# Performance work log

Hardware: AMD Instinct MI355X
Metric: run time of the kernel (lower is better)

The kernel has to match this reference:

```python
import jax, jax.numpy as jnp
import numpy as np

B, T, E, H = 2, 2048, 1024, 16  # batch, seq(block_size), n_embed, n_head


def setup_inputs() -> dict:
    key = jax.random.key(0)
    kx, kq, kk, kv, kf = jax.random.split(key, 5)
    s = 0.02
    return {
        "x": jax.random.normal(kx, (B, T, E), jnp.float32),
        "Wq": jax.random.normal(kq, (E, E), jnp.float32) * s,
        "Wk": jax.random.normal(kk, (E, E), jnp.float32) * s,
        "Wv": jax.random.normal(kv, (E, E), jnp.float32) * s,
        "Wf": jax.random.normal(kf, (E, E), jnp.float32) * s,
        "bf": jnp.zeros((E,), jnp.float32),
    }


def reference(x, Wq, Wk, Wv, Wf, bf):
    b, t, e = x.shape
    dh = e // H
    # per-head projections (no bias), heads concatenated along feature dim
    q = (x @ Wq).reshape(b, t, H, dh)
    k = (x @ Wk).reshape(b, t, H, dh)
    v = (x @ Wv).reshape(b, t, H, dh)
    # NOTE: original scales by sqrt(full embed dim C), not sqrt(head_size)
    scores = jnp.einsum("bqhd,bkhd->bhqk", q, k) / jnp.sqrt(jnp.asarray(e, x.dtype))
    causal = jnp.tril(jnp.ones((t, t), bool))
    scores = jnp.where(causal, scores, -jnp.inf)
    wei = jax.nn.softmax(scores, axis=-1)
    attn = jnp.einsum("bhqk,bkhd->bqhd", wei, v).reshape(b, t, e)
    x = x + attn  # residual (no out-projection in original)
    # FeedForward: single Linear + ReLU, residual
    return x + jnp.maximum(x @ Wf + bf, 0)
```

## Files before the change

### kernel.cpp

```cpp
#include <hip/hip_runtime.h>
#include <cstdint>
#include <cstddef>

typedef unsigned short u16;
typedef short short8 __attribute__((ext_vector_type(8)));
typedef float floatx4 __attribute__((ext_vector_type(4)));

__device__ __forceinline__ float bf2f(u16 u) {
    union { unsigned int i; float f; } v; v.i = ((unsigned int)u) << 16; return v.f;
}
__device__ __forceinline__ u16 f2bf(float f) {
    union { float f; unsigned int i; } v; v.f = f;
    unsigned int u = v.i;
    return (u16)((u + 0x7fffu + ((u >> 16) & 1u)) >> 16);
}

#if __has_builtin(__builtin_amdgcn_exp2f)
#define EXP2F(x) __builtin_amdgcn_exp2f(x)
#else
#define EXP2F(x) exp2f(x)
#endif

__device__ __forceinline__ void gload_lds16(const u16* g, void* lds_wave_base) {
    __builtin_amdgcn_global_load_lds(
        (__attribute__((address_space(1))) void*)g,
        (__attribute__((address_space(3))) void*)lds_wave_base,
        16, 0, 0);
}

__global__ void conv_transpose_k(const float* __restrict__ w0, const float* __restrict__ w1,
                                 const float* __restrict__ w2, const float* __restrict__ w3,
                                 u16* __restrict__ o0, u16* __restrict__ o1,
                                 u16* __restrict__ o2, u16* __restrict__ o3, int n) {
    __shared__ float t[32][33];
    const float* w; u16* o;
    switch (blockIdx.z) {
        case 0: w = w0; o = o0; break;
        case 1: w = w1; o = o1; break;
        case 2: w = w2; o = o2; break;
        default: w = w3; o = o3; break;
    }
    int tx = threadIdx.x, ty = threadIdx.y;
    int x0 = blockIdx.x * 32, y0 = blockIdx.y * 32;
    t[ty][tx] = w[(size_t)(y0 + ty) * n + x0 + tx];
    __syncthreads();
    o[(size_t)(x0 + ty) * n + y0 + tx] = f2bf(t[tx][ty]);
}

__global__ void conv_k(const float* __restrict__ in, u16* __restrict__ out, int n) {
    int i = (blockIdx.x * blockDim.x + threadIdx.x) * 4;
    if (i >= n) return;
    float4 v = *(const float4*)&in[i];
    ushort4 o;
    o.x = f2bf(v.x); o.y = f2bf(v.y); o.z = f2bf(v.z); o.w = f2bf(v.w);
    *(ushort4*)&out[i] = o;
}

#define QSTG(K0, BUF)                                                          \
    {                                                                          \
        _Pragma("unroll")                                                      \
        for (int it = 0; it < 2; ++it) {                                       \
            int idx = it * 256 + tid;                                          \
            int row = idx >> 2;                                                \
            int c8 = (idx & 3) * 8;                                            \
            size_t ldsoff = (size_t)(it * 256 + wave * 64) * 16;               \
            gload_lds16(&A[(size_t)(bm + row) * K + (K0) + c8],                \
                        (char*)smem + (BUF) * 8192 + ldsoff);                  \
            gload_lds16(&Bt[(size_t)(bn + row) * K + (K0) + c8],               \
                        (char*)smem + 16384 + (BUF) * 8192 + ldsoff);          \
        }                                                                      \
    }

__global__ __launch_bounds__(256) void gemm_qkv(
    const u16* __restrict__ A, const u16* __restrict__ Bt,
    u16* __restrict__ qpk, u16* __restrict__ kpk, u16* __restrict__ vpk,
    int M, int T, int K) {
    __shared__ __align__(16) u16 smem[16384];

    const int tid = threadIdx.x;
    const int lane = tid & 63, wave = tid >> 6;
    const int wm = (wave >> 1) * 64, wn = (wave & 1) * 64;
    const int bm = blockIdx.x * 128, bn = blockIdx.y * 128;
    const int l15 = lane & 15, lq = lane >> 4;

    const int sec = bn >> 10;
    u16* dst = (sec == 0) ? qpk : (sec == 1) ? kpk : vpk;
    const int bnE = bn & 1023;

    floatx4 acc[4][4];
#pragma unroll
    for (int i = 0; i < 4; ++i)
#pragma unroll
        for (int j = 0; j < 4; ++j) acc[i][j] = (floatx4)0.0f;

    const int nkt = K / 32;
    QSTG(0, 0);
    __syncthreads();

    for (int kt = 0; kt < nkt; ++kt) {
        const int cur = kt & 1;
        if (kt + 1 < nkt) QSTG((kt + 1) * 32, cur ^ 1);

        const u16* la = smem + cur * 4096;
        const u16* lb = smem + 8192 + cur * 4096;
        short8 af[4], bfr[4];
#pragma unroll
        for (int i = 0; i < 4; ++i) af[i] = *(const short8*)&la[(wm + i * 16 + l15) * 32 + lq * 8];
#pragma unroll
        for (int j = 0; j < 4; ++j) bfr[j] = *(const short8*)&lb[(wn + j * 16 + l15) * 32 + lq * 8];

#pragma unroll
        for (int i = 0; i < 4; ++i)
#pragma unroll
            for (int j = 0; j < 4; ++j)
                acc[i][j] = __builtin_amdgcn_mfma_f32_16x16x32_bf16(af[i], bfr[j], acc[i][j], 0, 0, 0);
        __syncthreads();
    }

    if (sec < 2) {
#pragma unroll
        for (int i = 0; i < 4; ++i)
#pragma unroll
            for (int r = 0; r < 4; ++r) {
                int trow = wm + i * 16 + lq * 4 + r;
                int s7 = ((trow >> 2) & 7) << 4;
#pragma unroll
                for (int j = 0; j < 4; ++j) {
                    int col = wn + j * 16 + l15;
                    smem[trow * 128 + (col ^ s7)] = f2bf(acc[i][j][r]);
                }
            }
        __syncthreads();
        const int rg = tid >> 3, cc = tid & 7;
#pragma unroll
        for (int p = 0; p < 4; ++p)
#pragma unroll
            for (int sfx = 0; sfx < 2; ++sfx) {
                int row = p * 32 + rg;
                int ch = cc + sfx * 8;
                short8 v = *(const short8*)&smem[row * 128 + ((ch * 8) ^ (((row >> 2) & 7) << 4))];
                int colE = bnE + ch * 8;
                int h = colE >> 6, d = colE & 63;
                int rowg = bm + row;
                int b = rowg >> 11, t = rowg & 2047;
                *(short8*)&dst[(((size_t)(b * 16 + h) * T) + t) * 64 + d] = v;
            }
    } else {
#pragma unroll
        for (int j = 0; j < 4; ++j) {
            int clo = wn + j * 16 + l15;
            int s7 = ((clo >> 2) & 7) << 4;
#pragma unroll
            for (int i = 0; i < 4; ++i)
#pragma unroll
                for (int r = 0; r < 4; ++r) {
                    int trow = wm + i * 16 + lq * 4 + r;
                    smem[clo * 128 + (trow ^ s7)] = f2bf(acc[i][j][r]);
                }
        }
        __syncthreads();
        const int rg = tid >> 3, cc = tid & 7;
        const int b = bm >> 11;
#pragma unroll
        for (int p = 0; p < 4; ++p)
#pragma unroll
            for (int sfx = 0; sfx < 2; ++sfx) {
                int clo = p * 32 + rg;
                int ch = cc + sfx * 8;
                short8 v = *(const short8*)&smem[clo * 128 + ((ch * 8) ^ (((clo >> 2) & 7) << 4))];
                int colE = bnE + clo;
                int h = colE >> 6, d = colE & 63;
                int t = (bm + ch * 8) & 2047;
                int kblk = t >> 6, tloc = t & 63;
                *(short8*)&dst[(((size_t)(b * 16 + h) * 32 + kblk) * 64 + d) * 64 + tloc] = v;
            }
    }
}

#define FSTG(K0, BUF)                                                          \
    {                                                                          \
        {                                                                      \
            int row = tid >> 2;                                                \
            int c8 = (tid & 3) * 8;                                            \
            size_t ldsoff = (size_t)(wave * 64) * 16;                          \
            gload_lds16(&A[(size_t)(bm + row) * K + (K0) + c8],                \
                        (char*)smemF + (BUF) * 4096 + ldsoff);                 \
        }                                                                      \
        _Pragma("unroll")                                                      \
        for (int it = 0; it < 2; ++it) {                                       \
            int idx = it * 256 + tid;                                          \
            int row = idx >> 2;                                                \
            int c8 = (idx & 3) * 8;                                            \
            size_t ldsoff = (size_t)(it * 256 + wave * 64) * 16;               \
            gload_lds16(&Bt[(size_t)(bn + row) * K + (K0) + c8],               \
                        (char*)smemF + 8192 + (BUF) * 8192 + ldsoff);          \
        }                                                                      \
    }

__global__ __launch_bounds__(256) void gemm64_bt(
    const u16* __restrict__ A, const u16* __restrict__ Bt, float* __restrict__ Cf,
    const float* __restrict__ bias, const u16* __restrict__ resid,
    int M, int N, int K) {
    __shared__ __align__(16) u16 smemF[12288];

    const int tid = threadIdx.x;
    const int lane = tid & 63, wave = tid >> 6;
    const int wm = (wave >> 1) * 32, wn = (wave & 1) * 64;
    const int bm = blockIdx.x * 64, bn = blockIdx.y * 128;
    const int l15 = lane & 15, lq = lane >> 4;

    floatx4 acc[2][4];
#pragma unroll
    for (int i = 0; i < 2; ++i)
#pragma unroll
        for (int j = 0; j < 4; ++j) acc[i][j] = (floatx4)0.0f;

    const int nkt = K / 32;
    FSTG(0, 0);
    __syncthreads();

    for (int kt = 0; kt < nkt; ++kt) {
        const int cur = kt & 1;
        if (kt + 1 < nkt) FSTG((kt + 1) * 32, cur ^ 1);

        const u16* la = smemF + cur * 2048;
        const u16* lb = smemF + 4096 + cur * 2048 * 2;
        short8 af[2], bfr[4];
#pragma unroll
        for (int i = 0; i < 2; ++i) af[i] = *(const short8*)&la[(wm + i * 16 + l15) * 32 + lq * 8];
#pragma unroll
        for (int j = 0; j < 4; ++j) bfr[j] = *(const short8*)&lb[(wn + j * 16 + l15) * 32 + lq * 8];

#pragma unroll
        for (int i = 0; i < 2; ++i)
#pragma unroll
            for (int j = 0; j < 4; ++j)
                acc[i][j] = __builtin_amdgcn_mfma_f32_16x16x32_bf16(af[i], bfr[j], acc[i][j], 0, 0, 0);
        __syncthreads();
    }

#pragma unroll
    for (int i = 0; i < 2; ++i)
#pragma unroll
        for (int j = 0; j < 4; ++j)
#pragma unroll
            for (int r = 0; r < 4; ++r) {
                int row = bm + wm + i * 16 + lq * 4 + r;
                int col = bn + wn + j * 16 + l15;
                float v = acc[i][j][r];
                v = fmaxf(v + bias[col], 0.0f) + bf2f(resid[(size_t)row * N + col]);
                Cf[(size_t)row * N + col] = v;
            }
}

#define STAGE(KT, BUF)                                                            \
    {                                                                             \
        const u16* kc_ = kb + (size_t)((KT) * 64 + r0) * 64 + swz0;               \
        gload_lds16(kc_, (char*)kbuf + (BUF) * 8192 + wave * 1024);               \
        gload_lds16(kc_ + 32 * 64, (char*)kbuf + (BUF) * 8192 + 4096 + wave * 1024); \
        const u16* vc_ = vp + (size_t)(KT) * 4096 + r0 * 64 + swz0;               \
        gload_lds16(vc_, (char*)vbuf + (BUF) * 8192 + wave * 1024);               \
        gload_lds16(vc_ + 32 * 64, (char*)vbuf + (BUF) * 8192 + 4096 + wave * 1024); \
    }

__global__ __launch_bounds__(256) void attn10_k(
    const u16* __restrict__ qpk, const u16* __restrict__ kpk,
    const u16* __restrict__ vpack, const float* __restrict__ xf,
    u16* __restrict__ y, int T, int E) {
    __shared__ u16 kbuf[2][64 * 64];
    __shared__ u16 vbuf[2][64 * 64];

    const int tid = threadIdx.x;
    const int lane = tid & 63, wave = tid >> 6;
    const int l15 = lane & 15, lq = lane >> 4;
    const int bh = blockIdx.x;
    const int b = bh >> 4, h = bh & 15;
    const int qb = 31 - (int)blockIdx.y;

    const u16* qp = qpk + (size_t)bh * T * 64;
    const u16* kb = kpk + (size_t)bh * T * 64;
    const u16* vp = vpack + (size_t)bh * T * 64;

    const float c2 = 0.04508422f;
    const int r0 = tid >> 3;
    const int slot = tid & 7;
    const int fr0 = (r0 & 3) | (((r0 >> 3) & 1) << 2);
    const int swz0 = ((slot - fr0) & 7) * 8;

    const int rbase = ((l15 >> 2) * 8) + (l15 & 3);
    const int sA = lq + (l15 & 7);
    const int sB = lq + ((l15 & 3) | (((l15 >> 3) & 1) << 2));

    const int qt = qb * 64 + wave * 16;
    const int qg = qt + l15;
    const int nkb = qb + 1;

    short8 aq[2];
#pragma unroll
    for (int c = 0; c < 2; ++c)
        aq[c] = *(const short8*)&qp[(size_t)qg * 64 + c * 32 + lq * 8];

    floatx4 o[4];
#pragma unroll
    for (int n = 0; n < 4; ++n) o[n] = (floatx4)0.0f;
    float lsum = 0.0f;

    STAGE(0, 0);
    __syncthreads();

#pragma unroll 1
    for (int kt = 0; kt < nkb; ++kt) {
        const int kc0 = kt * 64;
        const int cur = kt & 1;
        const int curoff = cur * 8192;

        if (kt + 1 < nkb) STAGE(kt + 1, cur ^ 1);

        floatx4 st[4];
        __builtin_amdgcn_s_setprio(1);
#pragma unroll
        for (int t2 = 0; t2 < 4; ++t2) {
            const int row = rbase + (t2 & 1) * 4 + (t2 >> 1) * 32;
            floatx4 sa = (floatx4)0.0f;
#pragma unroll
            for (int c = 0; c < 2; ++c) {
                int off = row * 128 + ((c * 4 + sA) & 7) * 16;
                short8 bk = *(const short8*)((const char*)kbuf + curoff + off);
                sa = __builtin_amdgcn_mfma_f32_16x16x32_bf16(bk, aq[c], sa, 0, 0, 0);
            }
            st[t2] = sa;
        }
        __builtin_amdgcn_s_setprio(0);

        const bool partial = (kt == qb);
        unsigned int pw[8];
#pragma unroll
        for (int t2 = 0; t2 < 4; ++t2) {
            float e0, e1, e2, e3;
            const int kg0 = kc0 + lq * 8 + (t2 & 1) * 4 + ((t2 >> 1) * 32);
            if (partial) {
                e0 = (kg0 + 0 <= qg) ? EXP2F(st[t2][0] * c2) : 0.0f;
                e1 = (kg0 + 1 <= qg) ? EXP2F(st[t2][1] * c2) : 0.0f;
                e2 = (kg0 + 2 <= qg) ? EXP2F(st[t2][2] * c2) : 0.0f;
                e3 = (kg0 + 3 <= qg) ? EXP2F(st[t2][3] * c2) : 0.0f;
            } else {
                e0 = EXP2F(st[t2][0] * c2);
                e1 = EXP2F(st[t2][1] * c2);
                e2 = EXP2F(st[t2][2] * c2);
                e3 = EXP2F(st[t2][3] * c2);
            }
            lsum += (e0 + e1) + (e2 + e3);
            unsigned int w0, w1;
            asm("v_cvt_pk_bf16_f32 %0, %1, %2" : "=v"(w0) : "v"(e0), "v"(e1));
            asm("v_cvt_pk_bf16_f32 %0, %1, %2" : "=v"(w1) : "v"(e2), "v"(e3));
            pw[t2 * 2 + 0] = w0;
            pw[t2 * 2 + 1] = w1;
        }

        __builtin_amdgcn_s_setprio(1);
#pragma unroll
        for (int kc = 0; kc < 2; ++kc) {
            union { unsigned int u[4]; short8 s; } ap;
            ap.u[0] = pw[kc * 4 + 0];
            ap.u[1] = pw[kc * 4 + 1];
            ap.u[2] = pw[kc * 4 + 2];
            ap.u[3] = pw[kc * 4 + 3];
#pragma unroll
            for (int n = 0; n < 4; ++n) {
                int off = (n * 16 + l15) * 128 + ((kc * 4 + sB) & 7) * 16;
                short8 bv = *(const short8*)((const char*)vbuf + curoff + off);
                o[n] = __builtin_amdgcn_mfma_f32_16x16x32_bf16(ap.s, bv, o[n], 0, 0, 0);
            }
        }
        __builtin_amdgcn_s_setprio(0);
        __syncthreads();
    }

    lsum += __shfl_xor(lsum, 16, 64);
    lsum += __shfl_xor(lsum, 32, 64);

    const float* xp = xf + (size_t)b * T * E + (size_t)h * 64;
    u16* yp = y + (size_t)b * T * E + (size_t)h * 64;
    float rl[4];
#pragma unroll
    for (int r = 0; r < 4; ++r) rl[r] = 1.0f / __shfl(lsum, lq * 4 + r, 64);
#pragma unroll
    for (int n = 0; n < 4; ++n)
#pragma unroll
        for (int r = 0; r < 4; ++r) {
            int rowg = qt + lq * 4 + r;
            int col = n * 16 + l15;
            float val = o[n][r] * rl[r];
            float res = __builtin_nontemporal_load(xp + (size_t)rowg * E + col);
            yp[(size_t)rowg * E + col] = f2bf(res + val);
        }
}

extern "C" void kernel_launch(void* const* d_in, const int* in_sizes, int n_in,
                              void* d_out, int out_size, void* d_ws, size_t ws_size,
                              hipStream_t stream) {
    const int B = 2, T = 2048, E = 1024;
    const int M = B * T;

    const float* x  = (const float*)d_in[0];
    const float* Wq = (const float*)d_in[1];
    const float* Wk = (const float*)d_in[2];
    const float* Wv = (const float*)d_in[3];
    const float* Wf = (const float*)d_in[4];
    const float* bf = (const float*)d_in[5];
    float* out = (float*)d_out;

    u16* ws = (u16*)d_ws;
    const size_t WN = (size_t)E * E;
    const size_t XN = (size_t)M * E;
    u16* Wqkv  = ws;
    u16* WfT   = ws + 3 * WN;
    u16* xb    = ws + 4 * WN;
    u16* qpk   = ws + 4 * WN + XN;
    u16* kpk   = ws + 4 * WN + 2 * XN;
    u16* vpk   = ws + 4 * WN + 3 * XN;
    u16* yb    = ws + 4 * WN + 4 * XN;

    conv_transpose_k<<<dim3(E / 32, E / 32, 4), dim3(32, 32), 0, stream>>>(
        Wq, Wk, Wv, Wf, Wqkv, Wqkv + WN, Wqkv + 2 * WN, WfT, E);
    conv_k<<<(int)(XN / 1024), 256, 0, stream>>>(x, xb, (int)XN);

    gemm_qkv<<<dim3(M / 128, 3 * E / 128), 256, 0, stream>>>(
        xb, Wqkv, qpk, kpk, vpk, M, T, E);

    attn10_k<<<dim3(B * 16, T / 64), 256, 0, stream>>>(qpk, kpk, vpk, x, yb, T, E);

    gemm64_bt<<<dim3(M / 64, E / 128), 256, 0, stream>>>(yb, WfT, out, bf, yb, M, E, E);
}
```

Measured before the change: 183.8 us.

## Use partial vmcnt waits and raw barriers to overlap prefetch with compute

```diff
diff --git a/kernel.cpp b/kernel.cpp
--- a/kernel.cpp
+++ b/kernel.cpp
@@ -27,6 +27,19 @@
         (__attribute__((address_space(3))) void*)lds_wave_base,
         16, 0, 0);
 }
+
+#define WAITVM(N) asm volatile("s_waitcnt vmcnt(" #N ")" ::: "memory")
+#define BARRIER_ACQ()                      \
+    do {                                   \
+        __builtin_amdgcn_s_barrier();      \
+        asm volatile("" ::: "memory");     \
+        __builtin_amdgcn_sched_barrier(0); \
+    } while (0)
+#define BARRIER_REL()                      \
+    do {                                   \
+        asm volatile("" ::: "memory");     \
+        __builtin_amdgcn_s_barrier();      \
+    } while (0)
 
 __global__ void conv_transpose_k(const float* __restrict__ w0, const float* __restrict__ w1,
                                  const float* __restrict__ w2, const float* __restrict__ w3,
@@ -71,7 +84,7 @@
         }                                                                      \
     }
 
-__global__ __launch_bounds__(256) void gemm_qkv(
+__global__ __launch_bounds__(256, 3) void gemm_qkv(
     const u16* __restrict__ A, const u16* __restrict__ Bt,
     u16* __restrict__ qpk, u16* __restrict__ kpk, u16* __restrict__ vpk,
     int M, int T, int K) {
@@ -95,11 +108,16 @@
 
     const int nkt = K / 32;
     QSTG(0, 0);
-    __syncthreads();
 
     for (int kt = 0; kt < nkt; ++kt) {
         const int cur = kt & 1;
-        if (kt + 1 < nkt) QSTG((kt + 1) * 32, cur ^ 1);
+        if (kt + 1 < nkt) {
+            QSTG((kt + 1) * 32, cur ^ 1);
+            WAITVM(4);
+        } else {
+            WAITVM(0);
+        }
+        BARRIER_ACQ();
 
         const u16* la = smem + cur * 4096;
         const u16* lb = smem + 8192 + cur * 4096;
@@ -114,7 +132,8 @@
 #pragma unroll
             for (int j = 0; j < 4; ++j)
                 acc[i][j] = __builtin_amdgcn_mfma_f32_16x16x32_bf16(af[i], bfr[j], acc[i][j], 0, 0, 0);
-        __syncthreads();
+
+        BARRIER_REL();
     }
 
     if (sec < 2) {
@@ -217,11 +236,16 @@
 
     const int nkt = K / 32;
     FSTG(0, 0);
-    __syncthreads();
 
     for (int kt = 0; kt < nkt; ++kt) {
         const int cur = kt & 1;
-        if (kt + 1 < nkt) FSTG((kt + 1) * 32, cur ^ 1);
+        if (kt + 1 < nkt) {
+            FSTG((kt + 1) * 32, cur ^ 1);
+            WAITVM(3);
+        } else {
+            WAITVM(0);
+        }
+        BARRIER_ACQ();
 
         const u16* la = smemF + cur * 2048;
         const u16* lb = smemF + 4096 + cur * 2048 * 2;
@@ -236,7 +260,8 @@
 #pragma unroll
             for (int j = 0; j < 4; ++j)
                 acc[i][j] = __builtin_amdgcn_mfma_f32_16x16x32_bf16(af[i], bfr[j], acc[i][j], 0, 0, 0);
-        __syncthreads();
+
+        BARRIER_REL();
     }
 
 #pragma unroll
@@ -263,7 +288,7 @@
         gload_lds16(vc_ + 32 * 64, (char*)vbuf + (BUF) * 8192 + 4096 + wave * 1024); \
     }
 
-__global__ __launch_bounds__(256) void attn10_k(
+__global__ __launch_bounds__(256) void attn11_k(
     const u16* __restrict__ qpk, const u16* __restrict__ kpk,
     const u16* __restrict__ vpack, const float* __restrict__ xf,
     u16* __restrict__ y, int T, int E) {
@@ -306,7 +331,6 @@
     float lsum = 0.0f;
 
     STAGE(0, 0);
-    __syncthreads();
 
 #pragma unroll 1
     for (int kt = 0; kt < nkb; ++kt) {
@@ -314,7 +338,13 @@
         const int cur = kt & 1;
         const int curoff = cur * 8192;
 
-        if (kt + 1 < nkb) STAGE(kt + 1, cur ^ 1);
+        if (kt + 1 < nkb) {
+            STAGE(kt + 1, cur ^ 1);
+            WAITVM(4);
+        } else {
+            WAITVM(0);
+        }
+        BARRIER_ACQ();
 
         floatx4 st[4];
         __builtin_amdgcn_s_setprio(1);
@@ -373,7 +403,8 @@
             }
         }
         __builtin_amdgcn_s_setprio(0);
-        __syncthreads();
+
+        BARRIER_REL();
     }
 
     lsum += __shfl_xor(lsum, 16, 64);
@@ -428,7 +459,7 @@
     gemm_qkv<<<dim3(M / 128, 3 * E / 128), 256, 0, stream>>>(
         xb, Wqkv, qpk, kpk, vpk, M, T, E);
 
-    attn10_k<<<dim3(B * 16, T / 64), 256, 0, stream>>>(qpk, kpk, vpk, x, yb, T, E);
+    attn11_k<<<dim3(B * 16, T / 64), 256, 0, stream>>>(qpk, kpk, vpk, x, yb, T, E);
 
     gemm64_bt<<<dim3(M / 64, E / 128), 256, 0, stream>>>(yb, WfT, out, bf, yb, M, E, E);
 }
```

Result: faster. 179.7 us (-2.2%).
